# Optimization experiments

Hardware: AMD Instinct MI355X
Metric: run time of the kernel (lower is better)

The kernel has to match this reference:

```python
import jax, jax.numpy as jnp
import numpy as np

BLOCK_SIZE = 64


def _dequant_weight(weight_packed, centroids, scales):
    # weight_packed: [out, in//2] bytes; each byte packs two 4-bit codes.
    # torch.cartesian_prod ordering: byte v -> (centroids[v >> 4], centroids[v & 0xF])
    hi = weight_packed >> 4
    lo = weight_packed & 0xF
    out_f, packed_in = weight_packed.shape
    w = jnp.stack([centroids[hi], centroids[lo]], axis=-1).reshape(out_f, packed_in * 2)
    num_blocks = scales.shape[1]
    w = (w.reshape(out_f, num_blocks, -1) * scales[:, :, None]).reshape(out_f, packed_in * 2)
    return w  # [out, in]


def setup_inputs() -> dict:
    key = jax.random.key(0)
    k1, k2, k3, k4 = jax.random.split(key, 4)
    B, S, IN, OUT = 2, 4096, 4096, 4096
    x = jax.random.normal(k1, (B, S, IN), dtype=jnp.float32)
    weight_packed = jax.random.randint(k2, (OUT, IN // 2), 0, 256, dtype=jnp.int32)
    centroids = jax.random.normal(k3, (16,), dtype=jnp.float32)
    scales = jax.random.uniform(k4, (OUT, IN // BLOCK_SIZE), dtype=jnp.float32)
    return {"x": x, "weight_packed": weight_packed, "centroids": centroids, "scales": scales}


def reference(x, weight_packed, centroids, scales):
    orig_shape = x.shape
    in_features = orig_shape[-1]
    x_flat = x.reshape(-1, in_features)  # [M, in]
    w = _dequant_weight(weight_packed, centroids, scales)  # [out, in]
    out = x_flat @ w.T  # [M, out]
    return out.reshape(*orig_shape[:-1], w.shape[0])
```

## Files before the change

kernel.cpp:

```cpp
#include <hip/hip_runtime.h>
#include <hip/hip_bf16.h>
#include <stdint.h>

typedef __bf16 bf16_t;
typedef bf16_t bf16x4 __attribute__((ext_vector_type(4)));
typedef bf16_t bf16x8 __attribute__((ext_vector_type(8)));
typedef float f32x4 __attribute__((ext_vector_type(4)));

#define GAS __attribute__((address_space(1)))
#define LAS __attribute__((address_space(3)))

__device__ __forceinline__ void async_load16(const void* g, void* l) {
    __builtin_amdgcn_global_load_lds((const GAS void*)g, (LAS void*)l, 16, 0, 0);
}

__global__ __launch_bounds__(256) void prep_kernel(
    const float* __restrict__ x, bf16_t* __restrict__ xb,
    const int* __restrict__ wp, const float* __restrict__ cen,
    const float* __restrict__ scl, bf16_t* __restrict__ W,
    int castBlocks, long nCastChunks, int nDeqChunks)
{
    if ((int)blockIdx.x < castBlocks) {
        long idx    = (long)blockIdx.x * blockDim.x + threadIdx.x;
        long stride = (long)castBlocks * blockDim.x;
        const float4* xv = (const float4*)x;
        bf16x8* xo = (bf16x8*)xb;
        for (long t = idx; t < nCastChunks; t += stride) {
            float4 a = xv[2 * t];
            float4 b = xv[2 * t + 1];
            bf16x8 o;
            o[0] = (bf16_t)a.x; o[1] = (bf16_t)a.y; o[2] = (bf16_t)a.z; o[3] = (bf16_t)a.w;
            o[4] = (bf16_t)b.x; o[5] = (bf16_t)b.y; o[6] = (bf16_t)b.z; o[7] = (bf16_t)b.w;
            xo[t] = o;
        }
    } else {
        __shared__ float c[16];
        if (threadIdx.x < 16) c[threadIdx.x] = cen[threadIdx.x];
        __syncthreads();
        int  nb     = (int)gridDim.x - castBlocks;
        long idx    = (long)((int)blockIdx.x - castBlocks) * blockDim.x + threadIdx.x;
        long stride = (long)nb * blockDim.x;
        const int4* wv = (const int4*)wp;
        bf16x8* wo = (bf16x8*)W;
        for (long t = idx; t < (long)nDeqChunks; t += stride) {
            int4 v = wv[t];
            long p   = t << 2;
            int  o   = (int)(p >> 11);
            int  pin = (int)p & 2047;
            float s = scl[(o << 6) + (pin >> 5)];
            int vv[4] = {v.x, v.y, v.z, v.w};
            bf16x8 outv;
#pragma unroll
            for (int i = 0; i < 4; ++i) {
                int b = vv[i];
                outv[2 * i]     = (bf16_t)(c[(b >> 4) & 15] * s);
                outv[2 * i + 1] = (bf16_t)(c[b & 15] * s);
            }
            wo[t] = outv;
        }
    }
}

#define BM 128
#define BN 128
#define BK 64

__global__ __launch_bounds__(256, 4) void gemm_bf16_nt(
    const bf16_t* __restrict__ A, const bf16_t* __restrict__ B,
    float* __restrict__ C, int M, int N, int K)
{
    __shared__ bf16_t lA[BM * BK];
    __shared__ bf16_t lB[BN * BK];

    const int tid  = threadIdx.x;
    const int wave = tid >> 6;
    const int lane = tid & 63;
    const int wm   = (wave >> 1) * 64;
    const int wn   = (wave & 1) * 64;

    const long m0 = (long)blockIdx.y * BM;
    const long n0 = (long)blockIdx.x * BN;

    const bf16_t* aP[4];
    const bf16_t* bP[4];
    int ldsOff[4];
#pragma unroll
    for (int r = 0; r < 4; ++r) {
        int s   = r * 256 + tid;
        int row = s >> 3;
        int kg  = (s & 7) ^ (row & 7);
        aP[r] = A + (m0 + row) * K + kg * 8;
        bP[r] = B + (n0 + row) * K + kg * 8;
        ldsOff[r] = (r * 256 + wave * 64) * 8;
    }

    const int qm = lane & 15;
    const int kcb = lane >> 4;
    const int swk = qm & 7;
    const bf16_t* pa = lA + (wm + qm) * BK;
    const bf16_t* pb = lB + (wn + qm) * BK;
    const int co0 = (kcb ^ swk) * 8;
    const int co1 = ((kcb + 4) ^ swk) * 8;

    f32x4 acc[4][4] = {};

    for (int k0 = 0; k0 < K; k0 += BK) {
#pragma unroll
        for (int r = 0; r < 4; ++r) async_load16(aP[r] + k0, lA + ldsOff[r]);
#pragma unroll
        for (int r = 0; r < 4; ++r) async_load16(bP[r] + k0, lB + ldsOff[r]);
        __syncthreads();

        bf16x8 af[4], bfv[4];
#pragma unroll
        for (int i = 0; i < 4; ++i) af[i] = *(const bf16x8*)(pa + i * 16 * BK + co0);
#pragma unroll
        for (int j = 0; j < 4; ++j) bfv[j] = *(const bf16x8*)(pb + j * 16 * BK + co0);
#pragma unroll
        for (int i = 0; i < 4; ++i)
#pragma unroll
            for (int j = 0; j < 4; ++j)
                acc[i][j] = __builtin_amdgcn_mfma_f32_16x16x32_bf16(af[i], bfv[j], acc[i][j], 0, 0, 0);
#pragma unroll
        for (int i = 0; i < 4; ++i) af[i] = *(const bf16x8*)(pa + i * 16 * BK + co1);
#pragma unroll
        for (int j = 0; j < 4; ++j) bfv[j] = *(const bf16x8*)(pb + j * 16 * BK + co1);
#pragma unroll
        for (int i = 0; i < 4; ++i)
#pragma unroll
            for (int j = 0; j < 4; ++j)
                acc[i][j] = __builtin_amdgcn_mfma_f32_16x16x32_bf16(af[i], bfv[j], acc[i][j], 0, 0, 0);
        __syncthreads();
    }

    const int crow = (lane >> 4) * 4;
    const int ccol = lane & 15;
#pragma unroll
    for (int i = 0; i < 4; ++i)
#pragma unroll
        for (int r = 0; r < 4; ++r) {
            float* cp = C + (m0 + wm + i * 16 + crow + r) * N + (n0 + wn + ccol);
#pragma unroll
            for (int j = 0; j < 4; ++j)
                cp[j * 16] = acc[i][j][r];
        }
}

__global__ void fallback_qgemm(const float* __restrict__ x, const int* __restrict__ wp,
                               const float* __restrict__ cen, const float* __restrict__ scl,
                               float* __restrict__ out, int M, int N, int Kp) {
    __shared__ float c[16];
    if (threadIdx.x < 16) c[threadIdx.x] = cen[threadIdx.x];
    __syncthreads();
    int n = blockIdx.x * blockDim.x + threadIdx.x;
    int m = blockIdx.y;
    if (n >= N) return;
    const float* xr = x + (long)m * (Kp * 2);
    const int*   wr = wp + (long)n * Kp;
    int nb = Kp / 32;
    float acc = 0.f;
    for (int b = 0; b < nb; ++b) {
        float s  = scl[n * nb + b];
        float pa = 0.f;
        for (int j = 0; j < 32; ++j) {
            int v = wr[b * 32 + j];
            pa += xr[(b * 32 + j) * 2]     * c[(v >> 4) & 15]
                + xr[(b * 32 + j) * 2 + 1] * c[v & 15];
        }
        acc += s * pa;
    }
    out[(long)m * N + n] = acc;
}

extern "C" void kernel_launch(void* const* d_in, const int* in_sizes, int n_in,
                              void* d_out, int out_size, void* d_ws, size_t ws_size,
                              hipStream_t stream) {
    const float* x   = (const float*)d_in[0];
    const int*   wp  = (const int*)d_in[1];
    const float* cen = (const float*)d_in[2];
    const float* scl = (const float*)d_in[3];
    float* out = (float*)d_out;

    const int  IN  = 4096;
    const int  OUT = 4096;
    const long M   = (long)in_sizes[0] / IN;

    size_t need = (size_t)(M * IN + (long)OUT * IN) * sizeof(bf16_t);
    if (ws_size >= need) {
        bf16_t* xb = (bf16_t*)d_ws;
        bf16_t* Wb = xb + M * IN;
        const int castBlocks = 2048;
        const int deqBlocks  = 512;
        long nCastChunks = M * IN / 8;
        int  nDeqChunks  = OUT * (IN / 2) / 4;
        prep_kernel<<<dim3(castBlocks + deqBlocks), dim3(256), 0, stream>>>(
            x, xb, wp, cen, scl, Wb, castBlocks, nCastChunks, nDeqChunks);
        dim3 grid(OUT / BN, (unsigned)(M / BM));
        gemm_bf16_nt<<<grid, dim3(256), 0, stream>>>(xb, Wb, out, (int)M, OUT, IN);
    } else {
        dim3 grid(OUT / 256, (unsigned)M);
        fallback_qgemm<<<grid, dim3(256), 0, stream>>>(x, wp, cen, scl, out, (int)M, OUT, IN / 2);
    }
}
```

Measured before the change: 499.5 us.

## Enlarge GEMM tile to 256x256 with double-buffered LDS prefetch and grid swizzle

Rewrites the bf16 GEMM to use 256x256 tiles with 8 waves, double-buffered LDS so the next K tile is loaded asynchronously while MFMAs run on the current one, raw s_barrier with explicit vmcnt waits, s_setprio around MFMA blocks, and a 1D grid with an XCD-aware block swizzle. The aim is to hide global-load latency behind compute and raise arithmetic intensity per tile loaded. LDS use grows to 128KB per block and each thread holds 128 accumulator floats, which limits occupancy and raises register pressure.

```diff
diff --git a/kernel.cpp b/kernel.cpp
--- a/kernel.cpp
+++ b/kernel.cpp
@@ -12,6 +12,12 @@
 
 __device__ __forceinline__ void async_load16(const void* g, void* l) {
     __builtin_amdgcn_global_load_lds((const GAS void*)g, (LAS void*)l, 16, 0, 0);
+}
+
+__device__ __forceinline__ void hw_barrier() {
+    asm volatile("" ::: "memory");
+    __builtin_amdgcn_s_barrier();
+    asm volatile("" ::: "memory");
 }
 
 __global__ __launch_bounds__(256) void prep_kernel(
@@ -61,88 +67,127 @@
     }
 }
 
-#define BM 128
-#define BN 128
+#define BM 256
+#define BN 256
 #define BK 64
 
-__global__ __launch_bounds__(256, 4) void gemm_bf16_nt(
+__global__ __launch_bounds__(512, 2) void gemm_bf16_nt(
     const bf16_t* __restrict__ A, const bf16_t* __restrict__ B,
     float* __restrict__ C, int M, int N, int K)
 {
-    __shared__ bf16_t lA[BM * BK];
-    __shared__ bf16_t lB[BN * BK];
+    __shared__ bf16_t lA[2][BM * BK];
+    __shared__ bf16_t lB[2][BN * BK];
 
     const int tid  = threadIdx.x;
     const int wave = tid >> 6;
     const int lane = tid & 63;
-    const int wm   = (wave >> 1) * 64;
-    const int wn   = (wave & 1) * 64;
-
-    const long m0 = (long)blockIdx.y * BM;
-    const long n0 = (long)blockIdx.x * BN;
-
-    const bf16_t* aP[4];
-    const bf16_t* bP[4];
-    int ldsOff[4];
+    const int wmB  = (wave >> 2) * 128;
+    const int wnB  = (wave & 3) * 64;
+
+    const int nwg = (int)gridDim.x;
+    const int cpx = nwg >> 3;
+    const int bid = (int)blockIdx.x;
+    const int swz = (bid & 7) * cpx + (bid >> 3);
+    const int nx  = N / BN;
+    const int by  = swz / nx;
+    const int bx  = swz - by * nx;
+    const long m0 = (long)by * BM;
+    const long n0 = (long)bx * BN;
+
+    int offA[4], offB[4], ldsOff[4];
 #pragma unroll
     for (int r = 0; r < 4; ++r) {
-        int s   = r * 256 + tid;
+        int s   = r * 512 + tid;
         int row = s >> 3;
         int kg  = (s & 7) ^ (row & 7);
-        aP[r] = A + (m0 + row) * K + kg * 8;
-        bP[r] = B + (n0 + row) * K + kg * 8;
-        ldsOff[r] = (r * 256 + wave * 64) * 8;
-    }
-
-    const int qm = lane & 15;
+        offA[r] = (int)(m0 + row) * K + kg * 8;
+        offB[r] = (int)(n0 + row) * K + kg * 8;
+        ldsOff[r] = (r * 512 + wave * 64) * 8;
+    }
+
+    auto stage = [&](int buf, int k0) {
+#pragma unroll
+        for (int r = 0; r < 4; ++r) async_load16(A + offA[r] + k0, &lA[buf][ldsOff[r]]);
+#pragma unroll
+        for (int r = 0; r < 4; ++r) async_load16(B + offB[r] + k0, &lB[buf][ldsOff[r]]);
+    };
+
+    const int qm  = lane & 15;
     const int kcb = lane >> 4;
-    const int swk = qm & 7;
-    const bf16_t* pa = lA + (wm + qm) * BK;
-    const bf16_t* pb = lB + (wn + qm) * BK;
-    const int co0 = (kcb ^ swk) * 8;
-    const int co1 = ((kcb + 4) ^ swk) * 8;
-
-    f32x4 acc[4][4] = {};
-
-    for (int k0 = 0; k0 < K; k0 += BK) {
-#pragma unroll
-        for (int r = 0; r < 4; ++r) async_load16(aP[r] + k0, lA + ldsOff[r]);
-#pragma unroll
-        for (int r = 0; r < 4; ++r) async_load16(bP[r] + k0, lB + ldsOff[r]);
-        __syncthreads();
-
-        bf16x8 af[4], bfv[4];
-#pragma unroll
-        for (int i = 0; i < 4; ++i) af[i] = *(const bf16x8*)(pa + i * 16 * BK + co0);
-#pragma unroll
-        for (int j = 0; j < 4; ++j) bfv[j] = *(const bf16x8*)(pb + j * 16 * BK + co0);
-#pragma unroll
-        for (int i = 0; i < 4; ++i)
-#pragma unroll
-            for (int j = 0; j < 4; ++j)
-                acc[i][j] = __builtin_amdgcn_mfma_f32_16x16x32_bf16(af[i], bfv[j], acc[i][j], 0, 0, 0);
-#pragma unroll
-        for (int i = 0; i < 4; ++i) af[i] = *(const bf16x8*)(pa + i * 16 * BK + co1);
-#pragma unroll
-        for (int j = 0; j < 4; ++j) bfv[j] = *(const bf16x8*)(pb + j * 16 * BK + co1);
-#pragma unroll
-        for (int i = 0; i < 4; ++i)
-#pragma unroll
-            for (int j = 0; j < 4; ++j)
-                acc[i][j] = __builtin_amdgcn_mfma_f32_16x16x32_bf16(af[i], bfv[j], acc[i][j], 0, 0, 0);
-        __syncthreads();
+    const int co0 = (kcb ^ (qm & 7)) * 8;
+    const int co1 = ((kcb + 4) ^ (qm & 7)) * 8;
+
+    f32x4 acc[8][4] = {};
+
+    stage(0, 0);
+    stage(1, BK);
+    asm volatile("s_waitcnt vmcnt(8)" ::: "memory");
+    hw_barrier();
+
+    const int NT = K / BK;
+    for (int j = 0; j < NT; ++j) {
+        const int c = j & 1;
+        const bf16_t* la = &lA[c][0];
+        const bf16_t* lb = &lB[c][0];
+
+        bf16x8 bfv[4][2], af[4][2];
+#pragma unroll
+        for (int nf = 0; nf < 4; ++nf) {
+            const bf16_t* pb = lb + (wnB + nf * 16 + qm) * BK;
+            bfv[nf][0] = *(const bf16x8*)(pb + co0);
+            bfv[nf][1] = *(const bf16x8*)(pb + co1);
+        }
+#pragma unroll
+        for (int mf = 0; mf < 4; ++mf) {
+            const bf16_t* pa = la + (wmB + mf * 16 + qm) * BK;
+            af[mf][0] = *(const bf16x8*)(pa + co0);
+            af[mf][1] = *(const bf16x8*)(pa + co1);
+        }
+        __builtin_amdgcn_s_setprio(1);
+#pragma unroll
+        for (int mf = 0; mf < 4; ++mf)
+#pragma unroll
+            for (int nf = 0; nf < 4; ++nf) {
+                acc[mf][nf] = __builtin_amdgcn_mfma_f32_16x16x32_bf16(af[mf][0], bfv[nf][0], acc[mf][nf], 0, 0, 0);
+                acc[mf][nf] = __builtin_amdgcn_mfma_f32_16x16x32_bf16(af[mf][1], bfv[nf][1], acc[mf][nf], 0, 0, 0);
+            }
+        __builtin_amdgcn_s_setprio(0);
+#pragma unroll
+        for (int mf = 0; mf < 4; ++mf) {
+            const bf16_t* pa = la + (wmB + (mf + 4) * 16 + qm) * BK;
+            af[mf][0] = *(const bf16x8*)(pa + co0);
+            af[mf][1] = *(const bf16x8*)(pa + co1);
+        }
+        __builtin_amdgcn_s_setprio(1);
+#pragma unroll
+        for (int mf = 0; mf < 4; ++mf)
+#pragma unroll
+            for (int nf = 0; nf < 4; ++nf) {
+                acc[mf + 4][nf] = __builtin_amdgcn_mfma_f32_16x16x32_bf16(af[mf][0], bfv[nf][0], acc[mf + 4][nf], 0, 0, 0);
+                acc[mf + 4][nf] = __builtin_amdgcn_mfma_f32_16x16x32_bf16(af[mf][1], bfv[nf][1], acc[mf + 4][nf], 0, 0, 0);
+            }
+        __builtin_amdgcn_s_setprio(0);
+
+        hw_barrier();
+        if (j + 2 < NT) {
+            stage(c, (j + 2) * BK);
+            asm volatile("s_waitcnt vmcnt(8)" ::: "memory");
+        } else if (j + 1 < NT) {
+            asm volatile("s_waitcnt vmcnt(0)" ::: "memory");
+        }
+        hw_barrier();
     }
 
     const int crow = (lane >> 4) * 4;
     const int ccol = lane & 15;
 #pragma unroll
-    for (int i = 0; i < 4; ++i)
+    for (int mf = 0; mf < 8; ++mf)
 #pragma unroll
         for (int r = 0; r < 4; ++r) {
-            float* cp = C + (m0 + wm + i * 16 + crow + r) * N + (n0 + wn + ccol);
-#pragma unroll
-            for (int j = 0; j < 4; ++j)
-                cp[j * 16] = acc[i][j][r];
+            float* cp = C + (m0 + wmB + mf * 16 + crow + r) * (long)N + (n0 + wnB + ccol);
+#pragma unroll
+            for (int nf = 0; nf < 4; ++nf)
+                cp[nf * 16] = acc[mf][nf][r];
         }
 }
 
@@ -186,7 +231,7 @@
     const long M   = (long)in_sizes[0] / IN;
 
     size_t need = (size_t)(M * IN + (long)OUT * IN) * sizeof(bf16_t);
-    if (ws_size >= need) {
+    if (ws_size >= need && (M % BM) == 0) {
         bf16_t* xb = (bf16_t*)d_ws;
         bf16_t* Wb = xb + M * IN;
         const int castBlocks = 2048;
@@ -195,8 +240,8 @@
         int  nDeqChunks  = OUT * (IN / 2) / 4;
         prep_kernel<<<dim3(castBlocks + deqBlocks), dim3(256), 0, stream>>>(
             x, xb, wp, cen, scl, Wb, castBlocks, nCastChunks, nDeqChunks);
-        dim3 grid(OUT / BN, (unsigned)(M / BM));
-        gemm_bf16_nt<<<grid, dim3(256), 0, stream>>>(xb, Wb, out, (int)M, OUT, IN);
+        int nwg = (OUT / BN) * (int)(M / BM);
+        gemm_bf16_nt<<<dim3(nwg), dim3(512), 0, stream>>>(xb, Wb, out, (int)M, OUT, IN);
     } else {
         dim3 grid(OUT / 256, (unsigned)M);
         fallback_qgemm<<<grid, dim3(256), 0, stream>>>(x, wp, cen, scl, out, (int)M, OUT, IN / 2);
```

Result: slower. 520.0 us (+4.1%).
